# Performance work log

Measured on AMD Instinct MI355X. Metric: run time of the kernel, lower is better.

Reference implementation:

```python
import jax, jax.numpy as jnp
import numpy as np

B, S, F = 16, 128, 64          # batch, seq_len, feature_dim
H = 256                        # hidden_dim
HEADS = 4
DH = H // HEADS                # GAT per-head dim = 64
AH = (2 * H) // HEADS          # temporal-attn head dim = 128
N = 1024                       # num graph nodes (edge_index.max()+1)
E = 16384                      # num edges (avg degree 16)
D2 = 2 * H                     # bi-LSTM output dim = 512
BN_INV = 1.0 / np.sqrt(1.0 + 1e-5)   # eval-mode BatchNorm1d (running mean=0, var=1)


def lstm_dir(x_sf, Wih, Whh, bih, bhh):
    # x_sf: [S, B, F]; torch gate order i, f, g, o
    h0 = jnp.zeros((x_sf.shape[1], Whh.shape[1]), x_sf.dtype)
    def step(carry, xt):
        h, c = carry
        z = xt @ Wih.T + h @ Whh.T + bih + bhh
        i, f, g, o = jnp.split(z, 4, axis=-1)
        c = jax.nn.sigmoid(f) * c + jax.nn.sigmoid(i) * jnp.tanh(g)
        h = jax.nn.sigmoid(o) * jnp.tanh(c)
        return (h, c), h
    _, hs = jax.lax.scan(step, (h0, h0), x_sf)
    return hs


def setup_inputs():
    key = jax.random.key(0)
    ks = jax.random.split(key, 32)
    g = lambda i, sh: jax.random.normal(ks[i], sh, jnp.float32) * 0.05
    return {
        "x": jax.random.normal(ks[0], (B, S, F), jnp.float32),
        "edge_index": jax.random.randint(ks[1], (2, E), 0, N),
        "Wih_f": g(2, (4 * H, F)), "Whh_f": g(3, (4 * H, H)),
        "bih_f": g(4, (4 * H,)), "bhh_f": g(5, (4 * H,)),
        "Wih_b": g(6, (4 * H, F)), "Whh_b": g(7, (4 * H, H)),
        "bih_b": g(8, (4 * H,)), "bhh_b": g(9, (4 * H,)),
        "Wq": g(10, (D2, D2)), "bq": g(11, (D2,)),
        "Wk": g(12, (D2, D2)), "bk": g(13, (D2,)),
        "Wv": g(14, (D2, D2)), "bv": g(15, (D2,)),
        "Wo": g(16, (D2, D2)), "bo": g(17, (D2,)),
        "W1": g(18, (D2, H)), "a1s": g(19, (HEADS, DH)), "a1d": g(20, (HEADS, DH)), "b1": g(21, (H,)),
        "g1": jnp.ones((H,), jnp.float32), "be1": jnp.zeros((H,), jnp.float32),
        "W2": g(22, (H, H)), "a2s": g(23, (HEADS, DH)), "a2d": g(24, (HEADS, DH)), "b2": g(25, (H,)),
        "g2": jnp.ones((H,), jnp.float32), "be2": jnp.zeros((H,), jnp.float32),
        "Wf": g(26, (H, 3 * H)), "bf": g(27, (H,)),
        "ln_g": jnp.ones((H,), jnp.float32), "ln_b": jnp.zeros((H,), jnp.float32),
    }


def reference(x, edge_index, Wih_f, Whh_f, bih_f, bhh_f, Wih_b, Whh_b, bih_b, bhh_b,
              Wq, bq, Wk, bk, Wv, bv, Wo, bo,
              W1, a1s, a1d, b1, g1, be1, W2, a2s, a2d, b2, g2, be2,
              Wf, bf, ln_g, ln_b):
    # ---- bidirectional LSTM ----
    xs = jnp.swapaxes(x, 0, 1)                                   # [S,B,F]
    hf = lstm_dir(xs, Wih_f, Whh_f, bih_f, bhh_f)
    hb = jnp.flip(lstm_dir(jnp.flip(xs, 0), Wih_b, Whh_b, bih_b, bhh_b), 0)
    t = jnp.swapaxes(jnp.concatenate([hf, hb], -1), 0, 1)        # [B,S,2H]
    # ---- temporal multi-head attention ----
    def proj(W, b):
        return (t @ W.T + b).reshape(B, S, HEADS, AH).transpose(0, 2, 1, 3)
    Q, K, V = proj(Wq, bq), proj(Wk, bk), proj(Wv, bv)
    scores = jnp.einsum('bhqd,bhkd->bhqk', Q, K) / np.sqrt(AH)
    attn = jax.nn.softmax(scores, -1)                            # [B,HEADS,S,S]
    ao = jnp.einsum('bhqk,bhkd->bhqd', attn, V).transpose(0, 2, 1, 3).reshape(B, S, D2)
    last = (ao @ Wo.T + bo)[:, -1, :]                            # [B,2H]
    # ---- 2-layer GAT per sample (PyG GATConv, add_self_loops=True), vmapped over batch ----
    loops = jnp.arange(N)
    src = jnp.concatenate([edge_index[0], loops])
    dst = jnp.concatenate([edge_index[1], loops])
    def gat(h_in, W, a_s, a_d, b):
        h = (h_in @ W).reshape(N, HEADS, DH)
        e = jax.nn.leaky_relu((h * a_s).sum(-1)[src] + (h * a_d).sum(-1)[dst], 0.2)  # [Etot,HEADS]
        m = jax.ops.segment_max(e, dst, num_segments=N)
        w = jnp.exp(e - m[dst])
        z = jax.ops.segment_sum(w, dst, num_segments=N)
        alpha = w / (z[dst] + 1e-16)
        out = jax.ops.segment_sum(alpha[:, :, None] * h[src], dst, num_segments=N)
        return out.reshape(N, H) + b
    def spatial(v):
        feat = jnp.broadcast_to(v, (N, D2))                      # uniform node features, per original
        h1 = jax.nn.elu(gat(feat, W1, a1s, a1d, b1) * BN_INV * g1 + be1)
        h2 = jax.nn.elu(gat(h1, W2, a2s, a2d, b2) * BN_INV * g2 + be2)
        return h2.mean(0)
    sp = jax.vmap(spatial)(last)                                 # [B,H]
    # ---- fusion: Linear + LayerNorm + ReLU (dropout = eval no-op) ----
    f = jnp.concatenate([last, sp], -1) @ Wf.T + bf
    mu = f.mean(-1, keepdims=True)
    var = ((f - mu) ** 2).mean(-1, keepdims=True)
    fused = jax.nn.relu((f - mu) / jnp.sqrt(var + 1e-5) * ln_g + ln_b)
    return fused, attn
```

## Files before the change

kernel.cpp:

```cpp
#include <hip/hip_runtime.h>


typedef unsigned short u16;
typedef unsigned int u32;
typedef __bf16 bf16x8 __attribute__((ext_vector_type(8)));
typedef float f32x4 __attribute__((ext_vector_type(4)));
typedef unsigned short ushort8v __attribute__((ext_vector_type(8)));
typedef unsigned int uint4v __attribute__((ext_vector_type(4)));

#define BN_INV_F 0.9999950000374997f
#define POISON 0xFFFFFFFFu

__device__ __forceinline__ float b2f(u16 u) {
  union { float f; unsigned int i; } v;
  v.i = ((unsigned int)u) << 16;
  return v.f;
}
__device__ __forceinline__ u16 f2b(float f) {
  union { float f; unsigned int i; } v;
  v.f = f;
  unsigned int x = v.i;
  unsigned int r = (x + 0x7FFFu + ((x >> 16) & 1u)) >> 16;
  return (u16)r;
}
__device__ __forceinline__ f32x4 mfma16(ushort8v a, ushort8v b, f32x4 c) {
  return __builtin_amdgcn_mfma_f32_16x16x32_bf16(
      __builtin_bit_cast(bf16x8, a), __builtin_bit_cast(bf16x8, b), c, 0, 0, 0);
}
__device__ __forceinline__ float sigm(float x) { return 1.f / (1.f + __expf(-x)); }
__device__ __forceinline__ float tanh_f(float x) {
  float e = __expf(2.f * x);
  return 1.f - 2.f / (e + 1.f);
}

__global__ __launch_bounds__(256) void lstm_kernel(
    const float* __restrict__ x,
    const float* __restrict__ Wih0, const float* __restrict__ Whh0,
    const float* __restrict__ bih0, const float* __restrict__ bhh0,
    const float* __restrict__ Wih1, const float* __restrict__ Whh1,
    const float* __restrict__ bih1, const float* __restrict__ bhh1,
    u32* __restrict__ hbuf,
    u16* __restrict__ tb)
{
  const int tid = threadIdx.x;
  const int bx = blockIdx.x;
  const int d = bx >> 4;
  const int q = bx & 15;
  const float* Wih = d ? Wih1 : Wih0;
  const float* Whh = d ? Whh1 : Whh0;
  const float* bih = d ? bih1 : bih0;
  const float* bhh = d ? bhh1 : bhh0;

  const int w = tid >> 6;
  const int ln = tid & 63;
  const int col16 = ln & 15;
  const int quad = ln >> 4;

  __shared__ u16 h_s[16][264];
  __shared__ u16 x_s[16][72];
  __shared__ float z_s[4][16][17];
  __shared__ float bias_s[64];

  const int G = w * 256 + q * 16 + col16;
  ushort8v whh_f[8];
#pragma unroll
  for (int kt = 0; kt < 8; kt++) {
    const float4* src = (const float4*)(Whh + G * 256 + kt * 32 + quad * 8);
    float4 v0 = src[0], v1 = src[1];
    ushort8v t8;
    t8[0] = f2b(v0.x); t8[1] = f2b(v0.y); t8[2] = f2b(v0.z); t8[3] = f2b(v0.w);
    t8[4] = f2b(v1.x); t8[5] = f2b(v1.y); t8[6] = f2b(v1.z); t8[7] = f2b(v1.w);
    whh_f[kt] = t8;
  }
  ushort8v wih_f[2];
#pragma unroll
  for (int kt = 0; kt < 2; kt++) {
    const float4* src = (const float4*)(Wih + G * 64 + kt * 32 + quad * 8);
    float4 v0 = src[0], v1 = src[1];
    ushort8v t8;
    t8[0] = f2b(v0.x); t8[1] = f2b(v0.y); t8[2] = f2b(v0.z); t8[3] = f2b(v0.w);
    t8[4] = f2b(v1.x); t8[5] = f2b(v1.y); t8[6] = f2b(v1.z); t8[7] = f2b(v1.w);
    wih_f[kt] = t8;
  }
  if (tid < 64) {
    int grow = ((tid >> 4) << 8) + q * 16 + (tid & 15);
    bias_s[tid] = bih[grow] + bhh[grow];
  }

  const int eb = tid >> 4;
  const int ec = tid & 15;
  float c_reg = 0.f;

  for (int t = 0; t < 128; t++) {
    const int pos = d ? (127 - t) : t;

    float4 xv = *(const float4*)(x + (eb * 128 + pos) * 64 + ec * 4);

    if (t > 0) {
      const u32* hw = hbuf + (t * 2 + d) * 2048 + tid * 8;
      uint4v a, b;
      for (;;) {
        asm volatile(
            "global_load_dwordx4 %0, %2, off sc1\n\t"
            "global_load_dwordx4 %1, %3, off sc1\n\t"
            "s_waitcnt vmcnt(0)"
            : "=v"(a), "=v"(b)
            : "v"(hw), "v"(hw + 4)
            : "memory");
        bool ok = (a.x != POISON) & (a.y != POISON) & (a.z != POISON) &
                  (a.w != POISON) & (b.x != POISON) & (b.y != POISON) &
                  (b.z != POISON) & (b.w != POISON);
        if (ok) break;
      }
      int b_ = tid >> 4, c0 = (tid & 15) * 16;
      *(u32*)&h_s[b_][c0 + 0] = a.x;
      *(u32*)&h_s[b_][c0 + 2] = a.y;
      *(u32*)&h_s[b_][c0 + 4] = a.z;
      *(u32*)&h_s[b_][c0 + 6] = a.w;
      *(u32*)&h_s[b_][c0 + 8] = b.x;
      *(u32*)&h_s[b_][c0 + 10] = b.y;
      *(u32*)&h_s[b_][c0 + 12] = b.z;
      *(u32*)&h_s[b_][c0 + 14] = b.w;
    }
    {
      int f0 = ec * 4;
      x_s[eb][f0 + 0] = f2b(xv.x);
      x_s[eb][f0 + 1] = f2b(xv.y);
      x_s[eb][f0 + 2] = f2b(xv.z);
      x_s[eb][f0 + 3] = f2b(xv.w);
    }
    __syncthreads();

    f32x4 acc = {0.f, 0.f, 0.f, 0.f};
#pragma unroll
    for (int kt = 0; kt < 2; kt++) {
      ushort8v av = *(const ushort8v*)&x_s[col16][kt * 32 + quad * 8];
      acc = mfma16(av, wih_f[kt], acc);
    }
    if (t > 0) {
#pragma unroll
      for (int kt = 0; kt < 8; kt++) {
        ushort8v av = *(const ushort8v*)&h_s[col16][kt * 32 + quad * 8];
        acc = mfma16(av, whh_f[kt], acc);
      }
    }
#pragma unroll
    for (int reg = 0; reg < 4; reg++)
      z_s[w][quad * 4 + reg][col16] = acc[reg];
    __syncthreads();

    float zi = z_s[0][eb][ec] + bias_s[ec];
    float zf = z_s[1][eb][ec] + bias_s[16 + ec];
    float zg = z_s[2][eb][ec] + bias_s[32 + ec];
    float zo = z_s[3][eb][ec] + bias_s[48 + ec];
    float si = sigm(zi), sf = sigm(zf), so = sigm(zo);
    float tg = tanh_f(zg);
    c_reg = sf * c_reg + si * tg;
    float hv = so * tanh_f(c_reg);
    u32 my = (u32)f2b(hv);
    u32 hi = __shfl_down((int)my, 1);
    if ((ec & 1) == 0) {
      u32 word = my | (hi << 16);
      *(u32*)&tb[(eb * 128 + pos) * 512 + d * 256 + q * 16 + ec] = word;
      if (t < 127) {
        u32* dst = hbuf + ((t + 1) * 2 + d) * 2048 + eb * 128 + (q * 16 + ec) / 2;
        __hip_atomic_store(dst, word, __ATOMIC_RELAXED,
                           __HIP_MEMORY_SCOPE_AGENT);
      }
    }
  }
}

__global__ __launch_bounds__(256) void qkv_kernel(
    const u16* __restrict__ tb,
    const float* __restrict__ Wq, const float* __restrict__ bq,
    const float* __restrict__ Wk, const float* __restrict__ bk,
    const float* __restrict__ Wv, const float* __restrict__ bv,
    u16* __restrict__ Qb, u16* __restrict__ Kb, u16* __restrict__ Vb)
{
  const int tid = threadIdx.x;
  const int bxm = blockIdx.x, byn = blockIdx.y, bz = blockIdx.z;
  const float* W = (bz == 0) ? Wq : ((bz == 1) ? Wk : Wv);
  const float* bias = (bz == 0) ? bq : ((bz == 1) ? bk : bv);
  u16* outp = (bz == 0) ? Qb : ((bz == 1) ? Kb : Vb);

  __shared__ u16 a_s[64][40];
  __shared__ u16 b_s[64][40];
  const int w = tid >> 6, ln = tid & 63, col16 = ln & 15, quad = ln >> 4;

  f32x4 acc[4];
#pragma unroll
  for (int n = 0; n < 4; n++) acc[n] = (f32x4){0.f, 0.f, 0.f, 0.f};

  for (int kt = 0; kt < 16; kt++) {
    int r = tid >> 2, seg = tid & 3;
    *(ushort8v*)&a_s[r][seg * 8] =
        *(const ushort8v*)(tb + (bxm * 64 + r) * 512 + kt * 32 + seg * 8);
    const float4* wsrc = (const float4*)(W + (byn * 64 + r) * 512 + kt * 32 + seg * 8);
    float4 w0 = wsrc[0], w1 = wsrc[1];
    b_s[r][seg * 8 + 0] = f2b(w0.x);
    b_s[r][seg * 8 + 1] = f2b(w0.y);
    b_s[r][seg * 8 + 2] = f2b(w0.z);
    b_s[r][seg * 8 + 3] = f2b(w0.w);
    b_s[r][seg * 8 + 4] = f2b(w1.x);
    b_s[r][seg * 8 + 5] = f2b(w1.y);
    b_s[r][seg * 8 + 6] = f2b(w1.z);
    b_s[r][seg * 8 + 7] = f2b(w1.w);
    __syncthreads();
    ushort8v av = *(const ushort8v*)&a_s[w * 16 + col16][quad * 8];
#pragma unroll
    for (int n = 0; n < 4; n++) {
      ushort8v bvv = *(const ushort8v*)&b_s[n * 16 + col16][quad * 8];
      acc[n] = mfma16(av, bvv, acc[n]);
    }
    __syncthreads();
  }
#pragma unroll
  for (int n = 0; n < 4; n++) {
    float bs = bias[byn * 64 + n * 16 + col16];
#pragma unroll
    for (int reg = 0; reg < 4; reg++) {
      int row = bxm * 64 + w * 16 + quad * 4 + reg;
      outp[row * 512 + byn * 64 + n * 16 + col16] = f2b(acc[n][reg] + bs);
    }
  }
}

__global__ __launch_bounds__(256) void attn_kernel(
    const u16* __restrict__ Qb, const u16* __restrict__ Kb,
    float* __restrict__ attn_out)
{
  const int b = blockIdx.x, h = blockIdx.y, half = blockIdx.z;
  const int tid = threadIdx.x;
  __shared__ __align__(16) char smem[52224];
  __shared__ float inv_s[64];
  u16 (*q_s)[136] = (u16(*)[136])smem;
  u16 (*k_s)[136] = (u16(*)[136])(smem + 17408);
  float (*sc)[132] = (float(*)[132])smem;

  const int w = tid >> 6, ln = tid & 63, col16 = ln & 15, quad = ln >> 4;
  {
    int r = tid >> 2, seg = tid & 3;
    const u16* src = Qb + (b * 128 + half * 64 + r) * 512 + h * 128 + seg * 32;
#pragma unroll
    for (int i = 0; i < 4; i++)
      *(ushort8v*)&q_s[r][seg * 32 + i * 8] = *(const ushort8v*)(src + i * 8);
    int r2 = tid >> 1, sg = tid & 1;
    const u16* src2 = Kb + (b * 128 + r2) * 512 + h * 128 + sg * 64;
#pragma unroll
    for (int i = 0; i < 8; i++)
      *(ushort8v*)&k_s[r2][sg * 64 + i * 8] = *(const ushort8v*)(src2 + i * 8);
  }
  __syncthreads();

  f32x4 acc[8];
#pragma unroll
  for (int n = 0; n < 8; n++) acc[n] = (f32x4){0.f, 0.f, 0.f, 0.f};
#pragma unroll
  for (int kd = 0; kd < 4; kd++) {
    ushort8v av = *(const ushort8v*)&q_s[w * 16 + col16][kd * 32 + quad * 8];
#pragma unroll
    for (int n = 0; n < 8; n++) {
      ushort8v bvv = *(const ushort8v*)&k_s[n * 16 + col16][kd * 32 + quad * 8];
      acc[n] = mfma16(av, bvv, acc[n]);
    }
  }
  __syncthreads();
  const float scale = 0.08838834764831845f;
#pragma unroll
  for (int n = 0; n < 8; n++)
#pragma unroll
    for (int reg = 0; reg < 4; reg++)
      sc[w * 16 + quad * 4 + reg][n * 16 + col16] = acc[n][reg] * scale;
  __syncthreads();

  const int row = tid >> 2, p = tid & 3;
  float m = -1e30f;
  for (int c0 = 0; c0 < 32; c0++) m = fmaxf(m, sc[row][p * 32 + c0]);
  m = fmaxf(m, __shfl_xor(m, 1));
  m = fmaxf(m, __shfl_xor(m, 2));
  float s = 0.f;
  for (int c0 = 0; c0 < 32; c0++) {
    float e = __expf(sc[row][p * 32 + c0] - m);
    sc[row][p * 32 + c0] = e;
    s += e;
  }
  s += __shfl_xor(s, 1);
  s += __shfl_xor(s, 2);
  if (p == 0) inv_s[row] = 1.f / s;
  __syncthreads();

  float* obase = attn_out + (size_t)((b * 4 + h) * 128 + half * 64) * 128;
#pragma unroll
  for (int it = 0; it < 8; it++) {
    int idx = tid + it * 256;
    int r = idx >> 5;
    int c4 = idx & 31;
    float4 ev = *(float4*)&sc[r][c4 * 4];
    float iv = inv_s[r];
    float4 ov = {ev.x * iv, ev.y * iv, ev.z * iv, ev.w * iv};
    *(float4*)&obase[r * 128 + c4 * 4] = ov;
  }
}

__global__ __launch_bounds__(256) void tail_kernel(
    const float* __restrict__ attn, const u16* __restrict__ Vb,
    const float* __restrict__ Wo, const float* __restrict__ bo,
    const float* __restrict__ W1, const float* __restrict__ b1,
    const float* __restrict__ g1, const float* __restrict__ be1,
    const float* __restrict__ W2, const float* __restrict__ pb2,
    const float* __restrict__ g2, const float* __restrict__ be2,
    const float* __restrict__ Wf, const float* __restrict__ bfv,
    const float* __restrict__ ln_g, const float* __restrict__ ln_b,
    float* __restrict__ dout)
{
  const int b = blockIdx.x, tid = threadIdx.x;
  __shared__ float arow[4][128];
  __shared__ float ao_s[512];
  __shared__ float last_s[512];
  __shared__ float h_s2[256];
  __shared__ float red_s[4];

#pragma unroll
  for (int e = 0; e < 2; e++) {
    int idx = tid + e * 256;
    int h = idx >> 7, k = idx & 127;
    arow[h][k] = attn[((b * 4 + h) * 128 + 127) * 128 + k];
  }
  __syncthreads();
#pragma unroll
  for (int pass = 0; pass < 2; pass++) {
    int d2 = tid + pass * 256;
    int hh = d2 >> 7;
    float acc = 0.f;
    for (int k = 0; k < 128; k++)
      acc += arow[hh][k] * b2f(Vb[(b * 128 + k) * 512 + d2]);
    ao_s[d2] = acc;
  }
  __syncthreads();
#pragma unroll
  for (int pass = 0; pass < 2; pass++) {
    int j = tid + pass * 256;
    float acc = bo[j];
    const float4* Wo4 = (const float4*)(Wo + j * 512);
    for (int k4 = 0; k4 < 128; k4++) {
      float4 wv = Wo4[k4];
      acc += ao_s[k4 * 4 + 0] * wv.x + ao_s[k4 * 4 + 1] * wv.y +
             ao_s[k4 * 4 + 2] * wv.z + ao_s[k4 * 4 + 3] * wv.w;
    }
    last_s[j] = acc;
  }
  __syncthreads();

  const int j = tid;
  float acc = 0.f;
  for (int k = 0; k < 512; k++) acc += last_s[k] * W1[k * 256 + j];
  float u = (acc + b1[j]) * BN_INV_F * g1[j] + be1[j];
  float h1 = u > 0.f ? u : expm1f(u);
  h_s2[j] = h1;
  __syncthreads();

  float acc2 = 0.f;
  for (int k = 0; k < 256; k++) acc2 += h_s2[k] * W2[k * 256 + j];
  float u2 = (acc2 + pb2[j]) * BN_INV_F * g2[j] + be2[j];
  float sp = u2 > 0.f ? u2 : expm1f(u2);
  __syncthreads();
  h_s2[j] = sp;
  __syncthreads();

  float f = bfv[j];
  const float4* Wf4 = (const float4*)(Wf + j * 768);
  for (int k4 = 0; k4 < 128; k4++) {
    float4 wv = Wf4[k4];
    f += last_s[k4 * 4 + 0] * wv.x + last_s[k4 * 4 + 1] * wv.y +
         last_s[k4 * 4 + 2] * wv.z + last_s[k4 * 4 + 3] * wv.w;
  }
  for (int k4 = 0; k4 < 64; k4++) {
    float4 wv = Wf4[128 + k4];
    f += h_s2[k4 * 4 + 0] * wv.x + h_s2[k4 * 4 + 1] * wv.y +
         h_s2[k4 * 4 + 2] * wv.z + h_s2[k4 * 4 + 3] * wv.w;
  }

  float v = f;
#pragma unroll
  for (int o = 32; o > 0; o >>= 1) v += __shfl_xor(v, o);
  if ((tid & 63) == 0) red_s[tid >> 6] = v;
  __syncthreads();
  float mu = (red_s[0] + red_s[1] + red_s[2] + red_s[3]) * (1.f / 256.f);
  float dv = f - mu;
  float vv = dv * dv;
#pragma unroll
  for (int o = 32; o > 0; o >>= 1) vv += __shfl_xor(vv, o);
  __syncthreads();
  if ((tid & 63) == 0) red_s[tid >> 6] = vv;
  __syncthreads();
  float var = (red_s[0] + red_s[1] + red_s[2] + red_s[3]) * (1.f / 256.f);
  float y = dv * rsqrtf(var + 1e-5f) * ln_g[j] + ln_b[j];
  dout[b * 256 + j] = fmaxf(y, 0.f);
}

extern "C" void kernel_launch(void* const* d_in, const int* in_sizes, int n_in,
                              void* d_out, int out_size, void* d_ws, size_t ws_size,
                              hipStream_t stream) {
  (void)in_sizes; (void)n_in; (void)out_size; (void)ws_size;
  const float* x     = (const float*)d_in[0];
  const float* Wih_f = (const float*)d_in[2];
  const float* Whh_f = (const float*)d_in[3];
  const float* bih_f = (const float*)d_in[4];
  const float* bhh_f = (const float*)d_in[5];
  const float* Wih_b = (const float*)d_in[6];
  const float* Whh_b = (const float*)d_in[7];
  const float* bih_b = (const float*)d_in[8];
  const float* bhh_b = (const float*)d_in[9];
  const float* Wq = (const float*)d_in[10]; const float* bq = (const float*)d_in[11];
  const float* Wk = (const float*)d_in[12]; const float* bk = (const float*)d_in[13];
  const float* Wv = (const float*)d_in[14]; const float* bv = (const float*)d_in[15];
  const float* Wo = (const float*)d_in[16]; const float* bo = (const float*)d_in[17];
  const float* W1 = (const float*)d_in[18];
  const float* b1 = (const float*)d_in[21];
  const float* g1 = (const float*)d_in[22]; const float* be1 = (const float*)d_in[23];
  const float* W2 = (const float*)d_in[24];
  const float* pb2 = (const float*)d_in[27];
  const float* g2 = (const float*)d_in[28]; const float* be2 = (const float*)d_in[29];
  const float* Wf = (const float*)d_in[30]; const float* bfv = (const float*)d_in[31];
  const float* ln_g = (const float*)d_in[32]; const float* ln_b = (const float*)d_in[33];

  float* dout = (float*)d_out;
  char* ws = (char*)d_ws;
  u32* hbuf = (u32*)(ws + 0);
  u16* tb   = (u16*)(ws + 2129920);
  u16* Qb   = (u16*)(ws + 4227072);
  u16* Kb   = (u16*)(ws + 6324224);
  u16* Vb   = (u16*)(ws + 8421376);

  (void)hipMemsetAsync(ws, 0xFF, 2097152, stream);
  lstm_kernel<<<32, 256, 0, stream>>>(x, Wih_f, Whh_f, bih_f, bhh_f,
                                      Wih_b, Whh_b, bih_b, bhh_b,
                                      hbuf, tb);
  qkv_kernel<<<dim3(32, 8, 3), 256, 0, stream>>>(tb, Wq, bq, Wk, bk, Wv, bv,
                                                 Qb, Kb, Vb);
  attn_kernel<<<dim3(16, 4, 2), 256, 0, stream>>>(Qb, Kb, dout + 4096);
  tail_kernel<<<16, 256, 0, stream>>>(dout + 4096, Vb, Wo, bo,
                                      W1, b1, g1, be1, W2, pb2, g2, be2,
                                      Wf, bfv, ln_g, ln_b, dout);
}
```

Measured before the change: 434.0 us.

## Pipeline LSTM hidden-state polling with multiple in-flight loads and split MFMA chains

Replaces the blocking poll loop that waited on each global load pair with hand-written assembly that keeps three load pairs in flight, rotates through them, and writes the first non-poison result straight to LDS. The hidden-state exchange buffer is relaid so each producer block's output is contiguous, the recurrent MFMA chain is split into two independent accumulators to shorten the dependency chain, and the global h store is issued before the tb output store. The aim is lower cross-block handoff latency on the sequential recurrence critical path. The cost is hardcoded VGPR clobbers and inline asm that can interfere with register allocation, plus extra polling memory traffic.

```diff
diff --git a/kernel.cpp b/kernel.cpp
--- a/kernel.cpp
+++ b/kernel.cpp
@@ -91,36 +91,82 @@
   const int ec = tid & 15;
   float c_reg = 0.f;
 
+  const unsigned lds_off =
+      (unsigned)(uintptr_t)(&h_s[tid >> 4][(tid & 15) * 16]);
+
   for (int t = 0; t < 128; t++) {
     const int pos = d ? (127 - t) : t;
 
     float4 xv = *(const float4*)(x + (eb * 128 + pos) * 64 + ec * 4);
 
     if (t > 0) {
-      const u32* hw = hbuf + (t * 2 + d) * 2048 + tid * 8;
-      uint4v a, b;
-      for (;;) {
-        asm volatile(
-            "global_load_dwordx4 %0, %2, off sc1\n\t"
-            "global_load_dwordx4 %1, %3, off sc1\n\t"
-            "s_waitcnt vmcnt(0)"
-            : "=v"(a), "=v"(b)
-            : "v"(hw), "v"(hw + 4)
-            : "memory");
-        bool ok = (a.x != POISON) & (a.y != POISON) & (a.z != POISON) &
-                  (a.w != POISON) & (b.x != POISON) & (b.y != POISON) &
-                  (b.z != POISON) & (b.w != POISON);
-        if (ok) break;
-      }
-      int b_ = tid >> 4, c0 = (tid & 15) * 16;
-      *(u32*)&h_s[b_][c0 + 0] = a.x;
-      *(u32*)&h_s[b_][c0 + 2] = a.y;
-      *(u32*)&h_s[b_][c0 + 4] = a.z;
-      *(u32*)&h_s[b_][c0 + 6] = a.w;
-      *(u32*)&h_s[b_][c0 + 8] = b.x;
-      *(u32*)&h_s[b_][c0 + 10] = b.y;
-      *(u32*)&h_s[b_][c0 + 12] = b.z;
-      *(u32*)&h_s[b_][c0 + 14] = b.w;
+      const u32* hw = hbuf + (t * 2 + d) * 2048 + (tid & 15) * 128 + (tid >> 4) * 8;
+      asm volatile(
+          "global_load_dwordx4 v[32:35], %[a0], off sc1\n\t"
+          "global_load_dwordx4 v[36:39], %[a1], off sc1\n\t"
+          "s_sleep 2\n\t"
+          "global_load_dwordx4 v[40:43], %[a0], off sc1\n\t"
+          "global_load_dwordx4 v[44:47], %[a1], off sc1\n\t"
+          "s_sleep 2\n\t"
+          "global_load_dwordx4 v[48:51], %[a0], off sc1\n\t"
+          "global_load_dwordx4 v[52:55], %[a1], off sc1\n\t"
+          "Lpoll_%=:\n\t"
+          "s_waitcnt vmcnt(4)\n\t"
+          "v_max_u32 v56, v32, v33\n\t"
+          "v_max_u32 v56, v56, v34\n\t"
+          "v_max_u32 v56, v56, v35\n\t"
+          "v_max_u32 v56, v56, v36\n\t"
+          "v_max_u32 v56, v56, v37\n\t"
+          "v_max_u32 v56, v56, v38\n\t"
+          "v_max_u32 v56, v56, v39\n\t"
+          "v_cmp_eq_u32 vcc, -1, v56\n\t"
+          "s_cbranch_vccz LdoneA_%=\n\t"
+          "global_load_dwordx4 v[32:35], %[a0], off sc1\n\t"
+          "global_load_dwordx4 v[36:39], %[a1], off sc1\n\t"
+          "s_waitcnt vmcnt(4)\n\t"
+          "v_max_u32 v56, v40, v41\n\t"
+          "v_max_u32 v56, v56, v42\n\t"
+          "v_max_u32 v56, v56, v43\n\t"
+          "v_max_u32 v56, v56, v44\n\t"
+          "v_max_u32 v56, v56, v45\n\t"
+          "v_max_u32 v56, v56, v46\n\t"
+          "v_max_u32 v56, v56, v47\n\t"
+          "v_cmp_eq_u32 vcc, -1, v56\n\t"
+          "s_cbranch_vccz LdoneB_%=\n\t"
+          "global_load_dwordx4 v[40:43], %[a0], off sc1\n\t"
+          "global_load_dwordx4 v[44:47], %[a1], off sc1\n\t"
+          "s_waitcnt vmcnt(4)\n\t"
+          "v_max_u32 v56, v48, v49\n\t"
+          "v_max_u32 v56, v56, v50\n\t"
+          "v_max_u32 v56, v56, v51\n\t"
+          "v_max_u32 v56, v56, v52\n\t"
+          "v_max_u32 v56, v56, v53\n\t"
+          "v_max_u32 v56, v56, v54\n\t"
+          "v_max_u32 v56, v56, v55\n\t"
+          "v_cmp_eq_u32 vcc, -1, v56\n\t"
+          "s_cbranch_vccz LdoneC_%=\n\t"
+          "global_load_dwordx4 v[48:51], %[a0], off sc1\n\t"
+          "global_load_dwordx4 v[52:55], %[a1], off sc1\n\t"
+          "s_branch Lpoll_%=\n\t"
+          "LdoneB_%=:\n\t"
+          "ds_write_b128 %[la], v[40:43]\n\t"
+          "ds_write_b128 %[la], v[44:47] offset:16\n\t"
+          "s_branch Lout_%=\n\t"
+          "LdoneC_%=:\n\t"
+          "ds_write_b128 %[la], v[48:51]\n\t"
+          "ds_write_b128 %[la], v[52:55] offset:16\n\t"
+          "s_branch Lout_%=\n\t"
+          "LdoneA_%=:\n\t"
+          "ds_write_b128 %[la], v[32:35]\n\t"
+          "ds_write_b128 %[la], v[36:39] offset:16\n\t"
+          "Lout_%=:\n\t"
+          :
+          : [a0] "v"(hw), [a1] "v"(hw + 4), [la] "v"(lds_off)
+          : "memory", "vcc",
+            "v32", "v33", "v34", "v35", "v36", "v37", "v38", "v39",
+            "v40", "v41", "v42", "v43", "v44", "v45", "v46", "v47",
+            "v48", "v49", "v50", "v51", "v52", "v53", "v54", "v55", "v56");
+      __builtin_amdgcn_sched_barrier(0);
     }
     {
       int f0 = ec * 4;
@@ -138,11 +184,16 @@
       acc = mfma16(av, wih_f[kt], acc);
     }
     if (t > 0) {
-#pragma unroll
-      for (int kt = 0; kt < 8; kt++) {
-        ushort8v av = *(const ushort8v*)&h_s[col16][kt * 32 + quad * 8];
-        acc = mfma16(av, whh_f[kt], acc);
+      f32x4 acc2 = {0.f, 0.f, 0.f, 0.f};
+#pragma unroll
+      for (int kt = 0; kt < 8; kt += 2) {
+        ushort8v av0 = *(const ushort8v*)&h_s[col16][kt * 32 + quad * 8];
+        ushort8v av1 = *(const ushort8v*)&h_s[col16][(kt + 1) * 32 + quad * 8];
+        acc = mfma16(av0, whh_f[kt], acc);
+        acc2 = mfma16(av1, whh_f[kt + 1], acc2);
       }
+      acc[0] += acc2[0]; acc[1] += acc2[1];
+      acc[2] += acc2[2]; acc[3] += acc2[3];
     }
 #pragma unroll
     for (int reg = 0; reg < 4; reg++)
@@ -161,12 +212,12 @@
     u32 hi = __shfl_down((int)my, 1);
     if ((ec & 1) == 0) {
       u32 word = my | (hi << 16);
-      *(u32*)&tb[(eb * 128 + pos) * 512 + d * 256 + q * 16 + ec] = word;
       if (t < 127) {
-        u32* dst = hbuf + ((t + 1) * 2 + d) * 2048 + eb * 128 + (q * 16 + ec) / 2;
+        u32* dst = hbuf + ((t + 1) * 2 + d) * 2048 + q * 128 + eb * 8 + (ec >> 1);
         __hip_atomic_store(dst, word, __ATOMIC_RELAXED,
                            __HIP_MEMORY_SCOPE_AGENT);
       }
+      *(u32*)&tb[(eb * 128 + pos) * 512 + d * 256 + q * 16 + ec] = word;
     }
   }
 }
```

New measurement: 494.0 us. +13.8%, slower.

## Spread LSTM blocks across XCDs and poll cached loads before coherent fallback

Applied to the files above, without the earlier changes.

Launches 128 LSTM blocks, of which only those with role 0/1 do work, so the 32 active blocks are mapped as forward/backward pairs by blockIdx low bits. This is likely meant to place them on particular XCDs or L2 slices. The h-polling loop now tries three loads with the sc0 cache policy before the sc1 load, and each producer also issues a plain store alongside the atomic store. The aim is lower latency on the per-timestep cross-block handoff, at the cost of relying on cache-coherence behaviour that may produce stale reads or wasted polling.

```diff
diff --git a/kernel.cpp b/kernel.cpp
--- a/kernel.cpp
+++ b/kernel.cpp
@@ -31,6 +31,11 @@
 __device__ __forceinline__ float tanh_f(float x) {
   float e = __expf(2.f * x);
   return 1.f - 2.f / (e + 1.f);
+}
+__device__ __forceinline__ bool ok8(const uint4v& a, const uint4v& b) {
+  return (a.x != POISON) & (a.y != POISON) & (a.z != POISON) &
+         (a.w != POISON) & (b.x != POISON) & (b.y != POISON) &
+         (b.z != POISON) & (b.w != POISON);
 }
 
 __global__ __launch_bounds__(256) void lstm_kernel(
@@ -44,8 +49,10 @@
 {
   const int tid = threadIdx.x;
   const int bx = blockIdx.x;
-  const int d = bx >> 4;
-  const int q = bx & 15;
+  const int role = bx & 7;
+  if (role > 1) return;
+  const int d = role;
+  const int q = bx >> 3;
   const float* Wih = d ? Wih1 : Wih0;
   const float* Whh = d ? Whh1 : Whh0;
   const float* bih = d ? bih1 : bih0;
@@ -87,6 +94,8 @@
     bias_s[tid] = bih[grow] + bhh[grow];
   }
 
+  __builtin_amdgcn_fence(__ATOMIC_ACQUIRE, "agent");
+
   const int eb = tid >> 4;
   const int ec = tid & 15;
   float c_reg = 0.f;
@@ -101,16 +110,29 @@
       uint4v a, b;
       for (;;) {
         asm volatile(
+            "global_load_dwordx4 %0, %2, off sc0\n\t"
+            "global_load_dwordx4 %1, %3, off sc0\n\t"
+            "s_waitcnt vmcnt(0)"
+            : "=v"(a), "=v"(b) : "v"(hw), "v"(hw + 4) : "memory");
+        if (ok8(a, b)) break;
+        asm volatile(
+            "global_load_dwordx4 %0, %2, off sc0\n\t"
+            "global_load_dwordx4 %1, %3, off sc0\n\t"
+            "s_waitcnt vmcnt(0)"
+            : "=v"(a), "=v"(b) : "v"(hw), "v"(hw + 4) : "memory");
+        if (ok8(a, b)) break;
+        asm volatile(
+            "global_load_dwordx4 %0, %2, off sc0\n\t"
+            "global_load_dwordx4 %1, %3, off sc0\n\t"
+            "s_waitcnt vmcnt(0)"
+            : "=v"(a), "=v"(b) : "v"(hw), "v"(hw + 4) : "memory");
+        if (ok8(a, b)) break;
+        asm volatile(
             "global_load_dwordx4 %0, %2, off sc1\n\t"
             "global_load_dwordx4 %1, %3, off sc1\n\t"
             "s_waitcnt vmcnt(0)"
-            : "=v"(a), "=v"(b)
-            : "v"(hw), "v"(hw + 4)
-            : "memory");
-        bool ok = (a.x != POISON) & (a.y != POISON) & (a.z != POISON) &
-                  (a.w != POISON) & (b.x != POISON) & (b.y != POISON) &
-                  (b.z != POISON) & (b.w != POISON);
-        if (ok) break;
+            : "=v"(a), "=v"(b) : "v"(hw), "v"(hw + 4) : "memory");
+        if (ok8(a, b)) break;
       }
       int b_ = tid >> 4, c0 = (tid & 15) * 16;
       *(u32*)&h_s[b_][c0 + 0] = a.x;
@@ -166,6 +188,8 @@
         u32* dst = hbuf + ((t + 1) * 2 + d) * 2048 + eb * 128 + (q * 16 + ec) / 2;
         __hip_atomic_store(dst, word, __ATOMIC_RELAXED,
                            __HIP_MEMORY_SCOPE_AGENT);
+        asm volatile("global_store_dword %0, %1, off"
+                     : : "v"(dst), "v"(word) : "memory");
       }
     }
   }
@@ -434,9 +458,9 @@
   u16* Vb   = (u16*)(ws + 8421376);
 
   (void)hipMemsetAsync(ws, 0xFF, 2097152, stream);
-  lstm_kernel<<<32, 256, 0, stream>>>(x, Wih_f, Whh_f, bih_f, bhh_f,
-                                      Wih_b, Whh_b, bih_b, bhh_b,
-                                      hbuf, tb);
+  lstm_kernel<<<128, 256, 0, stream>>>(x, Wih_f, Whh_f, bih_f, bhh_f,
+                                       Wih_b, Whh_b, bih_b, bhh_b,
+                                       hbuf, tb);
   qkv_kernel<<<dim3(32, 8, 3), 256, 0, stream>>>(tb, Wq, bq, Wk, bk, Wv, bv,
                                                  Qb, Kb, Vb);
   attn_kernel<<<dim3(16, 4, 2), 256, 0, stream>>>(Qb, Kb, dout + 4096);
```

New measurement: 667.3 us. 53.8% more time.

## Split each LSTM direction across two blocks instead of sixteen to cut cross-block sync

Applied to the files above, without the earlier changes.

The recurrent LSTM now runs on 4 blocks of 512 threads, two per direction, instead of 32 blocks of 256. Each block owns half the hidden units and keeps 4x more weight fragments in registers. Only the other block's half of h is spin-polled from global memory, and its own half is written straight to shared memory. This cuts the number of blocks that must synchronise each step through global poison-flag polling. In exchange each block does 4x more MFMA and gate work per step, and register pressure rises sharply.

```diff
diff --git a/kernel.cpp b/kernel.cpp
--- a/kernel.cpp
+++ b/kernel.cpp
@@ -6,7 +6,7 @@
 typedef __bf16 bf16x8 __attribute__((ext_vector_type(8)));
 typedef float f32x4 __attribute__((ext_vector_type(4)));
 typedef unsigned short ushort8v __attribute__((ext_vector_type(8)));
-typedef unsigned int uint4v __attribute__((ext_vector_type(4)));
+typedef unsigned int uint2v __attribute__((ext_vector_type(2)));
 
 #define BN_INV_F 0.9999950000374997f
 #define POISON 0xFFFFFFFFu
@@ -33,7 +33,7 @@
   return 1.f - 2.f / (e + 1.f);
 }
 
-__global__ __launch_bounds__(256) void lstm_kernel(
+__global__ __launch_bounds__(512) void lstm_kernel(
     const float* __restrict__ x,
     const float* __restrict__ Wih0, const float* __restrict__ Whh0,
     const float* __restrict__ bih0, const float* __restrict__ bhh0,
@@ -44,8 +44,9 @@
 {
   const int tid = threadIdx.x;
   const int bx = blockIdx.x;
-  const int d = bx >> 4;
-  const int q = bx & 15;
+  const int d = bx & 1;
+  const int p = bx >> 1;
+  const int op = 1 - p;
   const float* Wih = d ? Wih1 : Wih0;
   const float* Whh = d ? Whh1 : Whh0;
   const float* bih = d ? bih1 : bih0;
@@ -55,117 +56,130 @@
   const int ln = tid & 63;
   const int col16 = ln & 15;
   const int quad = ln >> 4;
+  const int g = w >> 1;
+  const int s = w & 1;
 
   __shared__ u16 h_s[16][264];
   __shared__ u16 x_s[16][72];
-  __shared__ float z_s[4][16][17];
-  __shared__ float bias_s[64];
-
-  const int G = w * 256 + q * 16 + col16;
-  ushort8v whh_f[8];
-#pragma unroll
-  for (int kt = 0; kt < 8; kt++) {
-    const float4* src = (const float4*)(Whh + G * 256 + kt * 32 + quad * 8);
-    float4 v0 = src[0], v1 = src[1];
-    ushort8v t8;
-    t8[0] = f2b(v0.x); t8[1] = f2b(v0.y); t8[2] = f2b(v0.z); t8[3] = f2b(v0.w);
-    t8[4] = f2b(v1.x); t8[5] = f2b(v1.y); t8[6] = f2b(v1.z); t8[7] = f2b(v1.w);
-    whh_f[kt] = t8;
-  }
-  ushort8v wih_f[2];
-#pragma unroll
-  for (int kt = 0; kt < 2; kt++) {
-    const float4* src = (const float4*)(Wih + G * 64 + kt * 32 + quad * 8);
-    float4 v0 = src[0], v1 = src[1];
-    ushort8v t8;
-    t8[0] = f2b(v0.x); t8[1] = f2b(v0.y); t8[2] = f2b(v0.z); t8[3] = f2b(v0.w);
-    t8[4] = f2b(v1.x); t8[5] = f2b(v1.y); t8[6] = f2b(v1.z); t8[7] = f2b(v1.w);
-    wih_f[kt] = t8;
-  }
-  if (tid < 64) {
-    int grow = ((tid >> 4) << 8) + q * 16 + (tid & 15);
-    bias_s[tid] = bih[grow] + bhh[grow];
-  }
-
-  const int eb = tid >> 4;
-  const int ec = tid & 15;
-  float c_reg = 0.f;
+  __shared__ float z_s[4][16][132];
+  __shared__ float bias_s[4][128];
+
+  ushort8v whh_f[4][8];
+  ushort8v wih_f[4][2];
+#pragma unroll
+  for (int nt = 0; nt < 4; nt++) {
+    const int G = g * 256 + p * 128 + s * 64 + nt * 16 + col16;
+#pragma unroll
+    for (int kt = 0; kt < 8; kt++) {
+      const float4* src = (const float4*)(Whh + G * 256 + kt * 32 + quad * 8);
+      float4 v0 = src[0], v1 = src[1];
+      ushort8v t8;
+      t8[0] = f2b(v0.x); t8[1] = f2b(v0.y); t8[2] = f2b(v0.z); t8[3] = f2b(v0.w);
+      t8[4] = f2b(v1.x); t8[5] = f2b(v1.y); t8[6] = f2b(v1.z); t8[7] = f2b(v1.w);
+      whh_f[nt][kt] = t8;
+    }
+#pragma unroll
+    for (int kt = 0; kt < 2; kt++) {
+      const float4* src = (const float4*)(Wih + G * 64 + kt * 32 + quad * 8);
+      float4 v0 = src[0], v1 = src[1];
+      ushort8v t8;
+      t8[0] = f2b(v0.x); t8[1] = f2b(v0.y); t8[2] = f2b(v0.z); t8[3] = f2b(v0.w);
+      t8[4] = f2b(v1.x); t8[5] = f2b(v1.y); t8[6] = f2b(v1.z); t8[7] = f2b(v1.w);
+      wih_f[nt][kt] = t8;
+    }
+  }
+  {
+    int gg = tid >> 7, cj = tid & 127;
+    int grow = gg * 256 + p * 128 + cj;
+    bias_s[gg][cj] = bih[grow] + bhh[grow];
+  }
+
+  const int eb = tid >> 5;
+  const int ec32 = tid & 31;
+  float c_reg[4] = {0.f, 0.f, 0.f, 0.f};
 
   for (int t = 0; t < 128; t++) {
     const int pos = d ? (127 - t) : t;
 
-    float4 xv = *(const float4*)(x + (eb * 128 + pos) * 64 + ec * 4);
+    const int xf = ec32 * 2;
+    float2 xv = *(const float2*)(x + (eb * 128 + pos) * 64 + xf);
 
     if (t > 0) {
-      const u32* hw = hbuf + (t * 2 + d) * 2048 + tid * 8;
-      uint4v a, b;
+      const u32* hw = hbuf + (t * 2 + d) * 2048 + eb * 128 + op * 64 + ec32 * 2;
+      uint2v a;
       for (;;) {
         asm volatile(
-            "global_load_dwordx4 %0, %2, off sc1\n\t"
-            "global_load_dwordx4 %1, %3, off sc1\n\t"
+            "global_load_dwordx2 %0, %1, off sc1\n\t"
             "s_waitcnt vmcnt(0)"
-            : "=v"(a), "=v"(b)
-            : "v"(hw), "v"(hw + 4)
-            : "memory");
-        bool ok = (a.x != POISON) & (a.y != POISON) & (a.z != POISON) &
-                  (a.w != POISON) & (b.x != POISON) & (b.y != POISON) &
-                  (b.z != POISON) & (b.w != POISON);
-        if (ok) break;
+            : "=v"(a) : "v"(hw) : "memory");
+        if ((a.x != POISON) & (a.y != POISON)) break;
       }
-      int b_ = tid >> 4, c0 = (tid & 15) * 16;
-      *(u32*)&h_s[b_][c0 + 0] = a.x;
-      *(u32*)&h_s[b_][c0 + 2] = a.y;
-      *(u32*)&h_s[b_][c0 + 4] = a.z;
-      *(u32*)&h_s[b_][c0 + 6] = a.w;
-      *(u32*)&h_s[b_][c0 + 8] = b.x;
-      *(u32*)&h_s[b_][c0 + 10] = b.y;
-      *(u32*)&h_s[b_][c0 + 12] = b.z;
-      *(u32*)&h_s[b_][c0 + 14] = b.w;
-    }
-    {
-      int f0 = ec * 4;
-      x_s[eb][f0 + 0] = f2b(xv.x);
-      x_s[eb][f0 + 1] = f2b(xv.y);
-      x_s[eb][f0 + 2] = f2b(xv.z);
-      x_s[eb][f0 + 3] = f2b(xv.w);
-    }
+      *(u32*)&h_s[eb][op * 128 + ec32 * 4 + 0] = a.x;
+      *(u32*)&h_s[eb][op * 128 + ec32 * 4 + 2] = a.y;
+    }
+    x_s[eb][xf + 0] = f2b(xv.x);
+    x_s[eb][xf + 1] = f2b(xv.y);
     __syncthreads();
 
-    f32x4 acc = {0.f, 0.f, 0.f, 0.f};
+    f32x4 acc[4];
+#pragma unroll
+    for (int nt = 0; nt < 4; nt++) acc[nt] = (f32x4){0.f, 0.f, 0.f, 0.f};
 #pragma unroll
     for (int kt = 0; kt < 2; kt++) {
       ushort8v av = *(const ushort8v*)&x_s[col16][kt * 32 + quad * 8];
-      acc = mfma16(av, wih_f[kt], acc);
+#pragma unroll
+      for (int nt = 0; nt < 4; nt++)
+        acc[nt] = mfma16(av, wih_f[nt][kt], acc[nt]);
     }
     if (t > 0) {
 #pragma unroll
       for (int kt = 0; kt < 8; kt++) {
         ushort8v av = *(const ushort8v*)&h_s[col16][kt * 32 + quad * 8];
-        acc = mfma16(av, whh_f[kt], acc);
+#pragma unroll
+        for (int nt = 0; nt < 4; nt++)
+          acc[nt] = mfma16(av, whh_f[nt][kt], acc[nt]);
       }
     }
 #pragma unroll
-    for (int reg = 0; reg < 4; reg++)
-      z_s[w][quad * 4 + reg][col16] = acc[reg];
+    for (int nt = 0; nt < 4; nt++)
+#pragma unroll
+      for (int reg = 0; reg < 4; reg++)
+        z_s[g][quad * 4 + reg][s * 64 + nt * 16 + col16] = acc[nt][reg];
     __syncthreads();
 
-    float zi = z_s[0][eb][ec] + bias_s[ec];
-    float zf = z_s[1][eb][ec] + bias_s[16 + ec];
-    float zg = z_s[2][eb][ec] + bias_s[32 + ec];
-    float zo = z_s[3][eb][ec] + bias_s[48 + ec];
-    float si = sigm(zi), sf = sigm(zf), so = sigm(zo);
-    float tg = tanh_f(zg);
-    c_reg = sf * c_reg + si * tg;
-    float hv = so * tanh_f(c_reg);
-    u32 my = (u32)f2b(hv);
-    u32 hi = __shfl_down((int)my, 1);
-    if ((ec & 1) == 0) {
-      u32 word = my | (hi << 16);
-      *(u32*)&tb[(eb * 128 + pos) * 512 + d * 256 + q * 16 + ec] = word;
+    u32 words[4];
+#pragma unroll
+    for (int j = 0; j < 4; j++) {
+      const int cj = j * 32 + ec32;
+      float zi = z_s[0][eb][cj] + bias_s[0][cj];
+      float zf = z_s[1][eb][cj] + bias_s[1][cj];
+      float zg = z_s[2][eb][cj] + bias_s[2][cj];
+      float zo = z_s[3][eb][cj] + bias_s[3][cj];
+      float si = sigm(zi), sf = sigm(zf), so = sigm(zo);
+      float tg = tanh_f(zg);
+      c_reg[j] = sf * c_reg[j] + si * tg;
+      float hv = so * tanh_f(c_reg[j]);
+      u32 my = (u32)f2b(hv);
+      h_s[eb][p * 128 + cj] = (u16)my;
+      u32 hi = ((u32)__shfl_down((int)my, 1)) & 0xFFFFu;
+      words[j] = my | (hi << 16);
+    }
+
+    if ((ec32 & 1) == 0) {
       if (t < 127) {
-        u32* dst = hbuf + ((t + 1) * 2 + d) * 2048 + eb * 128 + (q * 16 + ec) / 2;
-        __hip_atomic_store(dst, word, __ATOMIC_RELAXED,
-                           __HIP_MEMORY_SCOPE_AGENT);
+        const int slab = ((t + 1) * 2 + d) * 2048;
+#pragma unroll
+        for (int j = 0; j < 4; j++) {
+          const int cj = j * 32 + ec32;
+          u32* dst = hbuf + slab + eb * 128 + p * 64 + (cj >> 1);
+          __hip_atomic_store(dst, words[j], __ATOMIC_RELAXED,
+                             __HIP_MEMORY_SCOPE_AGENT);
+        }
+      }
+#pragma unroll
+      for (int j = 0; j < 4; j++) {
+        const int cj = j * 32 + ec32;
+        *(u32*)&tb[(eb * 128 + pos) * 512 + d * 256 + p * 128 + cj] = words[j];
       }
     }
   }
@@ -434,9 +448,9 @@
   u16* Vb   = (u16*)(ws + 8421376);
 
   (void)hipMemsetAsync(ws, 0xFF, 2097152, stream);
-  lstm_kernel<<<32, 256, 0, stream>>>(x, Wih_f, Whh_f, bih_f, bhh_f,
-                                      Wih_b, Whh_b, bih_b, bhh_b,
-                                      hbuf, tb);
+  lstm_kernel<<<4, 512, 0, stream>>>(x, Wih_f, Whh_f, bih_f, bhh_f,
+                                     Wih_b, Whh_b, bih_b, bhh_b,
+                                     hbuf, tb);
   qkv_kernel<<<dim3(32, 8, 3), 256, 0, stream>>>(tb, Wq, bq, Wk, bk, Wv, bv,
                                                  Qb, Kb, Vb);
   attn_kernel<<<dim3(16, 4, 2), 256, 0, stream>>>(Qb, Kb, dout + 4096);
```

New measurement: 631.8 us. 1.46x slower.
